# Kernel tuning notes

Hardware: AMD Instinct MI355X
Metric: run time of the kernel (lower is better)

Reference implementation:

```python
import jax, jax.numpy as jnp
import numpy as np

B, S, D = 4, 2048, 1024
H, N = 8, 16
HN = H * N
L = 2
DFF = 4 * D
V = 32000
C = 1024


def layer_norm(x, g, b, eps=1e-5):
    m = jnp.mean(x, axis=-1, keepdims=True)
    v = jnp.mean(jnp.square(x - m), axis=-1, keepdims=True)
    return (x - m) * jax.lax.rsqrt(v + eps) * g + b


def ssm_scan(alpha, b):
    # alpha, b: [B, S, H, N]; h_t = alpha_t * h_{t-1} + b_t
    h0 = jnp.zeros((alpha.shape[0], alpha.shape[2], alpha.shape[3]), alpha.dtype)

    def step(h, ab):
        a_t, b_t = ab
        h = a_t * h + b_t
        return h, h

    _, hs = jax.lax.scan(step, h0, (jnp.swapaxes(alpha, 0, 1), jnp.swapaxes(b, 0, 1)))
    return jnp.swapaxes(hs, 0, 1)  # [B, S, H, N]


def setup_inputs() -> dict:
    key = jax.random.key(0)
    ks = jax.random.split(key, 30)

    def rn(k, shape, std):
        return (jax.random.normal(k, shape, jnp.float32) * std).astype(jnp.float32)

    xav_d_hn = float(np.sqrt(6.0 / (D + HN)))
    xav_hn_d = float(np.sqrt(6.0 / (HN + D)))
    xav_d_ff = float(np.sqrt(6.0 / (D + DFF)))
    xav_ff_d = float(np.sqrt(6.0 / (DFF + D)))

    inp = {
        "x": jax.random.randint(ks[0], (B, S), 0, V),
        "emb": rn(ks[1], (V, D), 0.02),
        "pos_emb": rn(ks[2], (S, D), 0.02),
        # SSM layers (stacked over L). Weights stored [in, out].
        "alpha_W": rn(ks[3], (L, D, HN), 0.01),
        "alpha_b": jnp.full((L, HN), 2.0, jnp.float32),
        "in_W": jax.random.uniform(ks[4], (L, D, HN), jnp.float32, -xav_d_hn, xav_d_hn),
        "in_b": jnp.zeros((L, HN), jnp.float32),
        "out_W": jax.random.uniform(ks[5], (L, HN, D), jnp.float32, -xav_hn_d, xav_hn_d),
        "out_b": jnp.zeros((L, D), jnp.float32),
        "ssm_g": jnp.ones((L, D), jnp.float32),
        "ssm_beta": jnp.zeros((L, D), jnp.float32),
        # SwiGLU layers
        "w1_W": jax.random.uniform(ks[6], (L, D, DFF), jnp.float32, -xav_d_ff, xav_d_ff),
        "w1_b": jnp.zeros((L, DFF), jnp.float32),
        "w2_W": jax.random.uniform(ks[7], (L, DFF, D), jnp.float32, -xav_ff_d, xav_ff_d),
        "w2_b": jnp.zeros((L, D), jnp.float32),
        "w3_W": jax.random.uniform(ks[8], (L, D, DFF), jnp.float32, -xav_d_ff, xav_d_ff),
        "w3_b": jnp.zeros((L, DFF), jnp.float32),
        "ff_g": jnp.ones((L, D), jnp.float32),
        "ff_beta": jnp.zeros((L, D), jnp.float32),
        # output norm + head
        "on_g": jnp.ones((D,), jnp.float32),
        "on_beta": jnp.zeros((D,), jnp.float32),
        "h1_W": rn(ks[9], (D, 2 * D), 0.02),
        "h1_b": jnp.zeros((2 * D,), jnp.float32),
        "h2_W": rn(ks[10], (2 * D, C), 0.02),
        "h2_b": jnp.zeros((C,), jnp.float32),
    }
    return inp


def reference(x, emb, pos_emb, alpha_W, alpha_b, in_W, in_b, out_W, out_b,
              ssm_g, ssm_beta, w1_W, w1_b, w2_W, w2_b, w3_W, w3_b,
              ff_g, ff_beta, on_g, on_beta, h1_W, h1_b, h2_W, h2_b):
    b, s = x.shape
    h = emb[x] + pos_emb[:s][None, :, :]  # [B,S,D]
    for l in range(L):
        # DiagonalSSMLayer (dropout eval -> identity)
        xn = layer_norm(h, ssm_g[l], ssm_beta[l])
        alpha = jax.nn.sigmoid(xn @ alpha_W[l] + alpha_b[l]).reshape(b, s, H, N)
        bb = (xn @ in_W[l] + in_b[l]).reshape(b, s, H, N)
        hs = ssm_scan(alpha, bb).reshape(b, s, HN)
        h = h + hs @ out_W[l] + out_b[l]
        # SwiGLU block
        xn = layer_norm(h, ff_g[l], ff_beta[l])
        h = h + (jax.nn.silu(xn @ w1_W[l] + w1_b[l]) * (xn @ w3_W[l] + w3_b[l])) @ w2_W[l] + w2_b[l]
    h = layer_norm(h, on_g, on_beta)
    logits = jax.nn.gelu(h @ h1_W + h1_b, approximate=False) @ h2_W + h2_b
    return logits  # [B, S, C]
```

## Files before the change

### kernel.cpp

```cpp
#include <hip/hip_runtime.h>
#include <hip/hip_bf16.h>
#include <math.h>

#define B_    4
#define S_    2048
#define D_    1024
#define H_    8
#define N_    16
#define HN_   128
#define L_    2
#define DFF_  4096
#define C_    1024
#define MTOK  8192

using bf16 = __hip_bfloat16;
typedef __attribute__((ext_vector_type(8))) short  short8;
typedef __attribute__((ext_vector_type(4))) float  f32x4;

static __device__ __forceinline__ float sigmoidf_(float x) { return 1.f / (1.f + expf(-x)); }

static __device__ __forceinline__ unsigned short f2bf_bits(float f) {
    bf16 h = __float2bfloat16(f);
    return __builtin_bit_cast(unsigned short, h);
}

__global__ __launch_bounds__(256) void transpose_k(const float* __restrict__ src,
                                                   bf16* __restrict__ dst,
                                                   int K, int N) {
    __shared__ float t[32][33];
    int n0 = blockIdx.x * 32, k0 = blockIdx.y * 32;
    int tx = threadIdx.x, ty = threadIdx.y;
    #pragma unroll
    for (int i = ty; i < 32; i += 8)
        t[i][tx] = src[(size_t)(k0 + i) * N + n0 + tx];
    __syncthreads();
    #pragma unroll
    for (int i = ty; i < 32; i += 8)
        dst[(size_t)(n0 + i) * K + k0 + tx] = __float2bfloat16(t[tx][i]);
}

__global__ __launch_bounds__(256) void embed_k(const int* __restrict__ x,
                                               const float* __restrict__ emb,
                                               const float* __restrict__ pos,
                                               float* __restrict__ h) {
    int tok = blockIdx.x, t = threadIdx.x;
    int id = x[tok];
    int s  = tok & (S_ - 1);
    float4 a = ((const float4*)(emb + (size_t)id * D_))[t];
    float4 p = ((const float4*)(pos + (size_t)s * D_))[t];
    float4 r; r.x = a.x + p.x; r.y = a.y + p.y; r.z = a.z + p.z; r.w = a.w + p.w;
    ((float4*)(h + (size_t)tok * D_))[t] = r;
}

__global__ __launch_bounds__(256) void ln_k(const float* __restrict__ x,
                                            const float* __restrict__ g,
                                            const float* __restrict__ be,
                                            bf16* __restrict__ out) {
    int row = blockIdx.x, t = threadIdx.x;
    float4 v = ((const float4*)(x + (size_t)row * D_))[t];
    float s  = v.x + v.y + v.z + v.w;
    float sq = v.x * v.x + v.y * v.y + v.z * v.z + v.w * v.w;
    #pragma unroll
    for (int o = 32; o > 0; o >>= 1) {
        s  += __shfl_down(s, o);
        sq += __shfl_down(sq, o);
    }
    __shared__ float red[8];
    __shared__ float mv[2];
    int wave = t >> 6, lane = t & 63;
    if (lane == 0) { red[wave] = s; red[4 + wave] = sq; }
    __syncthreads();
    if (t == 0) {
        float S0 = red[0] + red[1] + red[2] + red[3];
        float Q  = red[4] + red[5] + red[6] + red[7];
        float m  = S0 * (1.f / 1024.f);
        float var = Q * (1.f / 1024.f) - m * m;
        mv[0] = m; mv[1] = rsqrtf(var + 1e-5f);
    }
    __syncthreads();
    float m = mv[0], rs = mv[1];
    float4 gg = ((const float4*)g)[t];
    float4 bb = ((const float4*)be)[t];
    ushort4 o;
    o.x = f2bf_bits((v.x - m) * rs * gg.x + bb.x);
    o.y = f2bf_bits((v.y - m) * rs * gg.y + bb.y);
    o.z = f2bf_bits((v.z - m) * rs * gg.z + bb.z);
    o.w = f2bf_bits((v.w - m) * rs * gg.w + bb.w);
    ((ushort4*)(out + (size_t)row * D_))[t] = o;
}

__global__ __launch_bounds__(256) void ssm_scan_k(const float* __restrict__ ab,
                                                  bf16* __restrict__ hs) {
    const int CL = S_ / 16;
    int bh = blockIdx.x;
    int b = bh >> 3, hh = bh & 7;
    int t = threadIdx.x;
    int chunk = t >> 4, n = t & 15;
    size_t rowbase = (size_t)b * S_ + (size_t)chunk * CL;
    const float* ap = ab + rowbase * 256 + hh * 16 + n;
    const float* bp = ap + 128;

    float A = 1.f, Bc = 0.f;
    for (int i = 0; i < CL; i++) {
        float a = ap[(size_t)i * 256], bv = bp[(size_t)i * 256];
        A *= a; Bc = a * Bc + bv;
    }
    __shared__ float sA[16][16], sB[16][16], sH[16][16];
    sA[chunk][n] = A; sB[chunk][n] = Bc;
    __syncthreads();
    if (t < 16) {
        float run = 0.f;
        #pragma unroll
        for (int c = 0; c < 16; c++) {
            sH[c][t] = run;
            run = sA[c][t] * run + sB[c][t];
        }
    }
    __syncthreads();
    float hrun = sH[chunk][n];
    bf16* op = hs + rowbase * 128 + hh * 16 + n;
    for (int i = 0; i < CL; i++) {
        float a = ap[(size_t)i * 256], bv = bp[(size_t)i * 256];
        hrun = a * hrun + bv;
        op[(size_t)i * 128] = __float2bfloat16(hrun);
    }
}

enum { EP_AB = 0, EP_BIAS_RES = 1, EP_BIAS_BF16 = 2, EP_SILUMUL_BF16 = 3,
       EP_GELU_BF16 = 4, EP_BIAS_F32 = 5 };

#define GLOAD_LDS(gp, lp) \
    __builtin_amdgcn_global_load_lds((__attribute__((address_space(1))) void*)(gp), \
                                     (__attribute__((address_space(3))) void*)(lp), 16, 0, 0)

template <int EP>
__global__ __launch_bounds__(256) void gemm_k(
    const bf16* __restrict__ A, const bf16* __restrict__ W,
    float* __restrict__ outF, bf16* __restrict__ outB,
    const float* __restrict__ b1, const float* __restrict__ b2,
    const float* __restrict__ resF, const bf16* __restrict__ resB,
    int M, int N, int K) {
    __shared__ __align__(16) bf16 As[128 * 64];
    __shared__ __align__(16) bf16 Bs[128 * 64];
    const int tid = threadIdx.x;
    const int wave = tid >> 6, lane = tid & 63;
    const int bm = blockIdx.x * 128, bn = blockIdx.y * 128;
    const int wr = (wave >> 1) * 64, wc = (wave & 1) * 64;

    f32x4 acc[4][4];
    #pragma unroll
    for (int m = 0; m < 4; m++)
        #pragma unroll
        for (int n = 0; n < 4; n++) acc[m][n] = f32x4{0.f, 0.f, 0.f, 0.f};

    const int srow = tid >> 3;
    const int skc  = (tid & 7) * 8;

    for (int k0 = 0; k0 < K; k0 += 64) {
        #pragma unroll
        for (int rr = 0; rr < 4; rr++) {
            int row = rr * 32 + srow;
            GLOAD_LDS(A + (size_t)(bm + row) * K + k0 + skc, As + row * 64 + skc);
            GLOAD_LDS(W + (size_t)(bn + row) * K + k0 + skc, Bs + row * 64 + skc);
        }
        __syncthreads();
        #pragma unroll
        for (int ks = 0; ks < 2; ks++) {
            const int kb = ks * 32 + (lane >> 4) * 8;
            short8 af[4], bfr[4];
            #pragma unroll
            for (int m = 0; m < 4; m++)
                af[m] = *reinterpret_cast<const short8*>(As + (wr + m * 16 + (lane & 15)) * 64 + kb);
            #pragma unroll
            for (int n = 0; n < 4; n++)
                bfr[n] = *reinterpret_cast<const short8*>(Bs + (wc + n * 16 + (lane & 15)) * 64 + kb);
            #pragma unroll
            for (int m = 0; m < 4; m++)
                #pragma unroll
                for (int n = 0; n < 4; n++)
                    acc[m][n] = __builtin_amdgcn_mfma_f32_16x16x32_bf16(af[m], bfr[n], acc[m][n], 0, 0, 0);
        }
        __syncthreads();
    }

    const int cb = bn + wc + (lane & 15);
    const int rb = bm + wr + (lane >> 4) * 4;
    #pragma unroll
    for (int m = 0; m < 4; m++) {
        #pragma unroll
        for (int n = 0; n < 4; n++) {
            int col = cb + n * 16;
            #pragma unroll
            for (int i = 0; i < 4; i++) {
                int row = rb + m * 16 + i;
                size_t idx = (size_t)row * N + col;
                float v = acc[m][n][i];
                if constexpr (EP == EP_AB) {
                    if (col < HN_) v = sigmoidf_(v + b1[col]);
                    else           v = v + b2[col - HN_];
                    outF[idx] = v;
                } else if constexpr (EP == EP_BIAS_RES) {
                    outF[idx] = v + b1[col] + resF[idx];
                } else if constexpr (EP == EP_BIAS_BF16) {
                    outB[idx] = __float2bfloat16(v + b1[col]);
                } else if constexpr (EP == EP_SILUMUL_BF16) {
                    float c1 = __bfloat162float(resB[idx]);
                    float sil = c1 * sigmoidf_(c1);
                    outB[idx] = __float2bfloat16((v + b1[col]) * sil);
                } else if constexpr (EP == EP_GELU_BF16) {
                    float xv = v + b1[col];
                    outB[idx] = __float2bfloat16(0.5f * xv * (1.f + erff(xv * 0.70710678118f)));
                } else {
                    outF[idx] = v + b1[col];
                }
            }
        }
    }
}

extern "C" void kernel_launch(void* const* d_in, const int* in_sizes, int n_in,
                              void* d_out, int out_size, void* d_ws, size_t ws_size,
                              hipStream_t stream) {
    const int*   x       = (const int*)  d_in[0];
    const float* emb     = (const float*)d_in[1];
    const float* pos_emb = (const float*)d_in[2];
    const float* alpha_W = (const float*)d_in[3];
    const float* alpha_b = (const float*)d_in[4];
    const float* in_W    = (const float*)d_in[5];
    const float* in_b    = (const float*)d_in[6];
    const float* out_W   = (const float*)d_in[7];
    const float* out_b   = (const float*)d_in[8];
    const float* ssm_g   = (const float*)d_in[9];
    const float* ssm_be  = (const float*)d_in[10];
    const float* w1_W    = (const float*)d_in[11];
    const float* w1_b    = (const float*)d_in[12];
    const float* w2_W    = (const float*)d_in[13];
    const float* w2_b    = (const float*)d_in[14];
    const float* w3_W    = (const float*)d_in[15];
    const float* w3_b    = (const float*)d_in[16];
    const float* ff_g    = (const float*)d_in[17];
    const float* ff_be   = (const float*)d_in[18];
    const float* on_g    = (const float*)d_in[19];
    const float* on_be   = (const float*)d_in[20];
    const float* h1_W    = (const float*)d_in[21];
    const float* h1_b    = (const float*)d_in[22];
    const float* h2_W    = (const float*)d_in[23];
    const float* h2_b    = (const float*)d_in[24];
    float* outp = (float*)d_out;
    (void)in_sizes; (void)n_in; (void)out_size; (void)ws_size;

    char* ws = (char*)d_ws;
    size_t off = 0;
    auto alloc = [&](size_t bytes) { size_t o = off; off += (bytes + 255) & ~(size_t)255; return o; };
    float* h    = (float*)(ws + alloc((size_t)MTOK * D_ * 4));
    bf16*  xn   = (bf16*) (ws + alloc((size_t)MTOK * D_ * 2));
    bf16*  abw  = (bf16*) (ws + alloc((size_t)L_ * 256 * D_ * 2));
    bf16*  outw = (bf16*) (ws + alloc((size_t)L_ * D_ * HN_ * 2));
    bf16*  w1w  = (bf16*) (ws + alloc((size_t)L_ * DFF_ * D_ * 2));
    bf16*  w3w  = (bf16*) (ws + alloc((size_t)L_ * DFF_ * D_ * 2));
    bf16*  w2w  = (bf16*) (ws + alloc((size_t)L_ * D_ * DFF_ * 2));
    bf16*  h1w  = (bf16*) (ws + alloc((size_t)2048 * D_ * 2));
    bf16*  h2w  = (bf16*) (ws + alloc((size_t)D_ * 2048 * 2));
    float* ab   = (float*)(ws + alloc((size_t)MTOK * 256 * 4));
    bf16*  hs   = (bf16*) (ws + alloc((size_t)MTOK * HN_ * 2));
    bf16*  c1   = (bf16*) (ws + alloc((size_t)MTOK * DFF_ * 2));

    auto T = [&](const float* src, bf16* dst, int K, int N) {
        transpose_k<<<dim3(N / 32, K / 32), dim3(32, 8), 0, stream>>>(src, dst, K, N);
    };

    for (int l = 0; l < L_; l++) {
        T(alpha_W + (size_t)l * D_ * HN_,  abw + (size_t)l * 256 * D_,                 D_,  HN_);
        T(in_W    + (size_t)l * D_ * HN_,  abw + (size_t)l * 256 * D_ + (size_t)HN_ * D_, D_, HN_);
        T(out_W   + (size_t)l * HN_ * D_,  outw + (size_t)l * D_ * HN_,                HN_, D_);
        T(w1_W    + (size_t)l * D_ * DFF_, w1w + (size_t)l * DFF_ * D_,                D_,  DFF_);
        T(w3_W    + (size_t)l * D_ * DFF_, w3w + (size_t)l * DFF_ * D_,                D_,  DFF_);
        T(w2_W    + (size_t)l * DFF_ * D_, w2w + (size_t)l * D_ * DFF_,                DFF_, D_);
    }
    T(h1_W, h1w, D_, 2048);
    T(h2_W, h2w, 2048, D_);

    embed_k<<<MTOK, 256, 0, stream>>>(x, emb, pos_emb, h);

    for (int l = 0; l < L_; l++) {
        ln_k<<<MTOK, 256, 0, stream>>>(h, ssm_g + l * D_, ssm_be + l * D_, xn);
        gemm_k<EP_AB><<<dim3(64, 2), 256, 0, stream>>>(
            xn, abw + (size_t)l * 256 * D_, ab, nullptr,
            alpha_b + l * HN_, in_b + l * HN_, nullptr, nullptr, MTOK, 256, D_);
        ssm_scan_k<<<B_ * H_, 256, 0, stream>>>(ab, hs);
        gemm_k<EP_BIAS_RES><<<dim3(64, 8), 256, 0, stream>>>(
            hs, outw + (size_t)l * D_ * HN_, h, nullptr,
            out_b + l * D_, nullptr, h, nullptr, MTOK, D_, HN_);
        ln_k<<<MTOK, 256, 0, stream>>>(h, ff_g + l * D_, ff_be + l * D_, xn);
        gemm_k<EP_BIAS_BF16><<<dim3(64, 32), 256, 0, stream>>>(
            xn, w1w + (size_t)l * DFF_ * D_, nullptr, c1,
            w1_b + l * DFF_, nullptr, nullptr, nullptr, MTOK, DFF_, D_);
        gemm_k<EP_SILUMUL_BF16><<<dim3(64, 32), 256, 0, stream>>>(
            xn, w3w + (size_t)l * DFF_ * D_, nullptr, c1,
            w3_b + l * DFF_, nullptr, nullptr, c1, MTOK, DFF_, D_);
        gemm_k<EP_BIAS_RES><<<dim3(64, 8), 256, 0, stream>>>(
            c1, w2w + (size_t)l * D_ * DFF_, h, nullptr,
            w2_b + l * D_, nullptr, h, nullptr, MTOK, D_, DFF_);
    }

    ln_k<<<MTOK, 256, 0, stream>>>(h, on_g, on_be, xn);
    gemm_k<EP_GELU_BF16><<<dim3(64, 16), 256, 0, stream>>>(
        xn, h1w, nullptr, c1, h1_b, nullptr, nullptr, nullptr, MTOK, 2048, D_);
    gemm_k<EP_BIAS_F32><<<dim3(64, 8), 256, 0, stream>>>(
        c1, h2w, outp, nullptr, h2_b, nullptr, nullptr, nullptr, MTOK, C_, 2048);
}
```

Baseline: 1.384 ms.

## Add 256-row tiled double-buffered GEMM kernel for the large projection matmuls

Adds a new GEMM kernel with 256x256 or 256x128 tiles and 512 threads. It uses XOR-swizzled LDS, direct global-to-LDS loads with explicit vmcnt waits, interleaved prefetch of the next tiles, setprio around the MFMA blocks, and a remapped block index for cache locality. The big FFN and head GEMMs move to this kernel to get more data reuse per tile and to overlap loads with compute. The trade-off is heavy dynamic LDS use (up to 128KB) and many hand-placed barriers, which lowers occupancy and makes correctness depend on exact wait counts.

```diff
diff --git a/kernel.cpp b/kernel.cpp
--- a/kernel.cpp
+++ b/kernel.cpp
@@ -23,6 +23,14 @@
     bf16 h = __float2bfloat16(f);
     return __builtin_bit_cast(unsigned short, h);
 }
+
+#define GLOAD_LDS(gp, lp) \
+    __builtin_amdgcn_global_load_lds((__attribute__((address_space(1))) void*)(gp), \
+                                     (__attribute__((address_space(3))) void*)(lp), 16, 0, 0)
+
+#define VMCNT(n) asm volatile("s_waitcnt vmcnt(" #n ")" ::: "memory")
+#define BARRIER() do { asm volatile("" ::: "memory"); __builtin_amdgcn_s_barrier(); \
+                       asm volatile("" ::: "memory"); } while (0)
 
 __global__ __launch_bounds__(256) void transpose_k(const float* __restrict__ src,
                                                    bf16* __restrict__ dst,
@@ -129,9 +137,31 @@
 enum { EP_AB = 0, EP_BIAS_RES = 1, EP_BIAS_BF16 = 2, EP_SILUMUL_BF16 = 3,
        EP_GELU_BF16 = 4, EP_BIAS_F32 = 5 };
 
-#define GLOAD_LDS(gp, lp) \
-    __builtin_amdgcn_global_load_lds((__attribute__((address_space(1))) void*)(gp), \
-                                     (__attribute__((address_space(3))) void*)(lp), 16, 0, 0)
+template <int EP>
+static __device__ __forceinline__ void ep_store(
+    float v, size_t idx, int col,
+    float* __restrict__ outF, bf16* __restrict__ outB,
+    const float* __restrict__ b1, const float* __restrict__ b2,
+    const float* __restrict__ resF, const bf16* __restrict__ resB) {
+    if constexpr (EP == EP_AB) {
+        if (col < HN_) v = sigmoidf_(v + b1[col]);
+        else           v = v + b2[col - HN_];
+        outF[idx] = v;
+    } else if constexpr (EP == EP_BIAS_RES) {
+        outF[idx] = v + b1[col] + resF[idx];
+    } else if constexpr (EP == EP_BIAS_BF16) {
+        outB[idx] = __float2bfloat16(v + b1[col]);
+    } else if constexpr (EP == EP_SILUMUL_BF16) {
+        float c1 = __bfloat162float(resB[idx]);
+        float sil = c1 * sigmoidf_(c1);
+        outB[idx] = __float2bfloat16((v + b1[col]) * sil);
+    } else if constexpr (EP == EP_GELU_BF16) {
+        float xv = v + b1[col];
+        outB[idx] = __float2bfloat16(0.5f * xv * (1.f + erff(xv * 0.70710678118f)));
+    } else {
+        outF[idx] = v + b1[col];
+    }
+}
 
 template <int EP>
 __global__ __launch_bounds__(256) void gemm_k(
@@ -186,36 +216,169 @@
     const int cb = bn + wc + (lane & 15);
     const int rb = bm + wr + (lane >> 4) * 4;
     #pragma unroll
-    for (int m = 0; m < 4; m++) {
+    for (int m = 0; m < 4; m++)
         #pragma unroll
         for (int n = 0; n < 4; n++) {
             int col = cb + n * 16;
             #pragma unroll
             for (int i = 0; i < 4; i++) {
                 int row = rb + m * 16 + i;
-                size_t idx = (size_t)row * N + col;
-                float v = acc[m][n][i];
-                if constexpr (EP == EP_AB) {
-                    if (col < HN_) v = sigmoidf_(v + b1[col]);
-                    else           v = v + b2[col - HN_];
-                    outF[idx] = v;
-                } else if constexpr (EP == EP_BIAS_RES) {
-                    outF[idx] = v + b1[col] + resF[idx];
-                } else if constexpr (EP == EP_BIAS_BF16) {
-                    outB[idx] = __float2bfloat16(v + b1[col]);
-                } else if constexpr (EP == EP_SILUMUL_BF16) {
-                    float c1 = __bfloat162float(resB[idx]);
-                    float sil = c1 * sigmoidf_(c1);
-                    outB[idx] = __float2bfloat16((v + b1[col]) * sil);
-                } else if constexpr (EP == EP_GELU_BF16) {
-                    float xv = v + b1[col];
-                    outB[idx] = __float2bfloat16(0.5f * xv * (1.f + erff(xv * 0.70710678118f)));
-                } else {
-                    outF[idx] = v + b1[col];
-                }
+                ep_store<EP>(acc[m][n][i], (size_t)row * N + col, col,
+                             outF, outB, b1, b2, resF, resB);
             }
         }
-    }
+}
+
+extern __shared__ __align__(16) char smem_g256[];
+
+template <int BN, int EP>
+__global__ __launch_bounds__(512, 2) void gemm256_k(
+    const bf16* __restrict__ A, const bf16* __restrict__ W,
+    float* __restrict__ outF, bf16* __restrict__ outB,
+    const float* __restrict__ b1, const float* __restrict__ b2,
+    const float* __restrict__ resF, const bf16* __restrict__ resB,
+    int M, int N, int K) {
+    constexpr int NR   = BN / 64;
+    constexpr int NBJ  = BN / 64;
+    constexpr int WCS  = NR * 16;
+    constexpr int ASZB = 256 * 64 * 2;
+    constexpr int BSZB = BN * 64 * 2;
+    constexpr int BUFB = ASZB + BSZB;
+
+    const int tid = threadIdx.x;
+    const int wid = tid >> 6, lane = tid & 63;
+    const int wr = wid >> 2, wc = wid & 3;
+    const int l15 = lane & 15, l4 = lane >> 4;
+    const int swz = (lane & 7) << 4;
+
+    const int nwg = gridDim.x;
+    const int bid = ((int)blockIdx.x & 7) * (nwg >> 3) + ((int)blockIdx.x >> 3);
+    const int gx = M >> 8;
+    const int bm = (bid % gx) * 256;
+    const int bn = (bid / gx) * BN;
+
+    const int nt = K >> 6;
+
+    auto stageA = [&](int t, int j) {
+        int c = tid + (j << 9);
+        int row = c >> 3;
+        int cc = (c & 7) ^ (row & 7);
+        GLOAD_LDS(A + (size_t)(bm + row) * K + t * 64 + cc * 8,
+                  smem_g256 + (size_t)(t & 1) * BUFB + (size_t)c * 16);
+    };
+    auto stageB = [&](int t, int j) {
+        int c = tid + (j << 9);
+        int row = c >> 3;
+        int cc = (c & 7) ^ (row & 7);
+        GLOAD_LDS(W + (size_t)(bn + row) * K + t * 64 + cc * 8,
+                  smem_g256 + (size_t)(t & 1) * BUFB + ASZB + (size_t)c * 16);
+    };
+    auto rdA = [&](int b, int m, int ks) -> short8 {
+        int off = b * BUFB + ((wr * 128 + m * 16 + l15) << 7) + (((ks << 6) + (l4 << 4)) ^ swz);
+        return *reinterpret_cast<const short8*>(smem_g256 + off);
+    };
+    auto rdB = [&](int b, int n, int ks) -> short8 {
+        int off = b * BUFB + ASZB + ((wc * WCS + n * 16 + l15) << 7) + (((ks << 6) + (l4 << 4)) ^ swz);
+        return *reinterpret_cast<const short8*>(smem_g256 + off);
+    };
+
+    f32x4 acc[8][NR];
+    #pragma unroll
+    for (int m = 0; m < 8; m++)
+        #pragma unroll
+        for (int n = 0; n < NR; n++) acc[m][n] = f32x4{0.f, 0.f, 0.f, 0.f};
+
+    #pragma unroll
+    for (int j = 0; j < 4; j++) stageA(0, j);
+    #pragma unroll
+    for (int j = 0; j < NBJ; j++) stageB(0, j);
+    #pragma unroll
+    for (int j = 0; j < 4; j++) stageA(1, j);
+    #pragma unroll
+    for (int j = 0; j < NBJ; j++) stageB(1, j);
+
+    short8 aF[4], bF[NR][2];
+
+    for (int v = 0; v < nt; ++v) {
+        const int b = v & 1;
+        if (v == 0)            { if constexpr (BN == 256) VMCNT(8); else VMCNT(6); }
+        else if (v + 1 < nt)   { if constexpr (BN == 256) VMCNT(6); else VMCNT(4); }
+        else                   VMCNT(0);
+        BARRIER();
+
+        #pragma unroll
+        for (int m = 0; m < 4; m++) aF[m] = rdA(b, m, 0);
+        #pragma unroll
+        for (int n = 0; n < NR; n++) bF[n][0] = rdB(b, n, 0);
+        if (v >= 1 && v + 1 < nt) { stageA(v + 1, 1); stageA(v + 1, 3); }
+        BARRIER();
+        __builtin_amdgcn_s_setprio(1);
+        #pragma unroll
+        for (int m = 0; m < 4; m++)
+            #pragma unroll
+            for (int n = 0; n < NR; n++)
+                acc[m][n] = __builtin_amdgcn_mfma_f32_16x16x32_bf16(aF[m], bF[n][0], acc[m][n], 0, 0, 0);
+        __builtin_amdgcn_s_setprio(0);
+        BARRIER();
+
+        #pragma unroll
+        for (int m = 0; m < 4; m++) aF[m] = rdA(b, m, 1);
+        #pragma unroll
+        for (int n = 0; n < NR; n++) bF[n][1] = rdB(b, n, 1);
+        BARRIER();
+        __builtin_amdgcn_s_setprio(1);
+        #pragma unroll
+        for (int m = 0; m < 4; m++)
+            #pragma unroll
+            for (int n = 0; n < NR; n++)
+                acc[m][n] = __builtin_amdgcn_mfma_f32_16x16x32_bf16(aF[m], bF[n][1], acc[m][n], 0, 0, 0);
+        __builtin_amdgcn_s_setprio(0);
+        BARRIER();
+
+        #pragma unroll
+        for (int m = 0; m < 4; m++) aF[m] = rdA(b, 4 + m, 0);
+        if (v + 2 < nt) {
+            #pragma unroll
+            for (int j = 0; j < NBJ; j++) stageB(v + 2, j);
+            stageA(v + 2, 0); stageA(v + 2, 2);
+        }
+        BARRIER();
+        __builtin_amdgcn_s_setprio(1);
+        #pragma unroll
+        for (int m = 0; m < 4; m++)
+            #pragma unroll
+            for (int n = 0; n < NR; n++)
+                acc[4 + m][n] = __builtin_amdgcn_mfma_f32_16x16x32_bf16(aF[m], bF[n][0], acc[4 + m][n], 0, 0, 0);
+        __builtin_amdgcn_s_setprio(0);
+        BARRIER();
+
+        #pragma unroll
+        for (int m = 0; m < 4; m++) aF[m] = rdA(b, 4 + m, 1);
+        BARRIER();
+        __builtin_amdgcn_s_setprio(1);
+        #pragma unroll
+        for (int m = 0; m < 4; m++)
+            #pragma unroll
+            for (int n = 0; n < NR; n++)
+                acc[4 + m][n] = __builtin_amdgcn_mfma_f32_16x16x32_bf16(aF[m], bF[n][1], acc[4 + m][n], 0, 0, 0);
+        __builtin_amdgcn_s_setprio(0);
+        BARRIER();
+    }
+
+    const int gc0 = bn + wc * WCS + l15;
+    const int gr0 = bm + wr * 128 + l4 * 4;
+    #pragma unroll
+    for (int m = 0; m < 8; m++)
+        #pragma unroll
+        for (int n = 0; n < NR; n++) {
+            int col = gc0 + n * 16;
+            #pragma unroll
+            for (int i = 0; i < 4; i++) {
+                int row = gr0 + m * 16 + i;
+                ep_store<EP>(acc[m][n][i], (size_t)row * N + col, col,
+                             outF, outB, b1, b2, resF, resB);
+            }
+        }
 }
 
 extern "C" void kernel_launch(void* const* d_in, const int* in_sizes, int n_in,
@@ -249,6 +412,12 @@
     float* outp = (float*)d_out;
     (void)in_sizes; (void)n_in; (void)out_size; (void)ws_size;
 
+    hipFuncSetAttribute((const void*)gemm256_k<256, EP_BIAS_BF16>,   hipFuncAttributeMaxDynamicSharedMemorySize, 131072);
+    hipFuncSetAttribute((const void*)gemm256_k<256, EP_SILUMUL_BF16>,hipFuncAttributeMaxDynamicSharedMemorySize, 131072);
+    hipFuncSetAttribute((const void*)gemm256_k<256, EP_GELU_BF16>,   hipFuncAttributeMaxDynamicSharedMemorySize, 131072);
+    hipFuncSetAttribute((const void*)gemm256_k<128, EP_BIAS_RES>,    hipFuncAttributeMaxDynamicSharedMemorySize, 98304);
+    hipFuncSetAttribute((const void*)gemm256_k<128, EP_BIAS_F32>,    hipFuncAttributeMaxDynamicSharedMemorySize, 98304);
+
     char* ws = (char*)d_ws;
     size_t off = 0;
     auto alloc = [&](size_t bytes) { size_t o = off; off += (bytes + 255) & ~(size_t)255; return o; };
@@ -292,20 +461,20 @@
             hs, outw + (size_t)l * D_ * HN_, h, nullptr,
             out_b + l * D_, nullptr, h, nullptr, MTOK, D_, HN_);
         ln_k<<<MTOK, 256, 0, stream>>>(h, ff_g + l * D_, ff_be + l * D_, xn);
-        gemm_k<EP_BIAS_BF16><<<dim3(64, 32), 256, 0, stream>>>(
+        gemm256_k<256, EP_BIAS_BF16><<<dim3(32 * (DFF_ / 256)), 512, 131072, stream>>>(
             xn, w1w + (size_t)l * DFF_ * D_, nullptr, c1,
             w1_b + l * DFF_, nullptr, nullptr, nullptr, MTOK, DFF_, D_);
-        gemm_k<EP_SILUMUL_BF16><<<dim3(64, 32), 256, 0, stream>>>(
+        gemm256_k<256, EP_SILUMUL_BF16><<<dim3(32 * (DFF_ / 256)), 512, 131072, stream>>>(
             xn, w3w + (size_t)l * DFF_ * D_, nullptr, c1,
             w3_b + l * DFF_, nullptr, nullptr, c1, MTOK, DFF_, D_);
-        gemm_k<EP_BIAS_RES><<<dim3(64, 8), 256, 0, stream>>>(
+        gemm256_k<128, EP_BIAS_RES><<<dim3(32 * (D_ / 128)), 512, 98304, stream>>>(
             c1, w2w + (size_t)l * D_ * DFF_, h, nullptr,
             w2_b + l * D_, nullptr, h, nullptr, MTOK, D_, DFF_);
     }
 
     ln_k<<<MTOK, 256, 0, stream>>>(h, on_g, on_be, xn);
-    gemm_k<EP_GELU_BF16><<<dim3(64, 16), 256, 0, stream>>>(
+    gemm256_k<256, EP_GELU_BF16><<<dim3(32 * (2048 / 256)), 512, 131072, stream>>>(
         xn, h1w, nullptr, c1, h1_b, nullptr, nullptr, nullptr, MTOK, 2048, D_);
-    gemm_k<EP_BIAS_F32><<<dim3(64, 8), 256, 0, stream>>>(
+    gemm256_k<128, EP_BIAS_F32><<<dim3(32 * (C_ / 128)), 512, 98304, stream>>>(
         c1, h2w, outp, nullptr, h2_b, nullptr, nullptr, nullptr, MTOK, C_, 2048);
 }
```

Measured after the change: 1.154 ms. -16.7%, faster.
